# Kernel tuning notes

Measured on AMD Instinct MI355X. Metric: run time of the kernel, lower is better.

The kernel has to match this reference:

```python
import jax, jax.numpy as jnp
import numpy as np

VOCAB = 100000
EMB = 100
HID = 100
CTX_LEN = 60          # must equal MAX_DESC_LEN for linear_1 to fit
FACT_LEN = 20
DESC_LEN = 60


def setup_inputs() -> dict:
    key = jax.random.key(0)
    ks = jax.random.split(key, 12)
    s = 0.05
    context = jax.random.randint(ks[0], (CTX_LEN, FACT_LEN), 1, VOCAB)
    fact_lengths = jax.random.randint(ks[1], (CTX_LEN,), 1, FACT_LEN)
    description = jax.random.randint(ks[2], (DESC_LEN,), 1, VOCAB)
    emb_ctx = jax.random.normal(ks[3], (VOCAB, EMB), jnp.float32) * s
    emb_ctx = emb_ctx.at[0].set(0.0)  # padding_idx=0
    emb_dec = jax.random.normal(ks[4], (VOCAB, EMB), jnp.float32) * s
    emb_dec = emb_dec.at[0].set(0.0)
    w1 = jax.random.normal(ks[5], (HID, CTX_LEN * HID), jnp.float32) * s
    b1 = jax.random.normal(ks[6], (HID,), jnp.float32) * s
    w_ih = jax.random.normal(ks[7], (3 * HID, EMB), jnp.float32) * s
    w_hh = jax.random.normal(ks[8], (3 * HID, HID), jnp.float32) * s
    b_ih = jax.random.normal(ks[9], (3 * HID,), jnp.float32) * s
    b_hh = jax.random.normal(ks[10], (3 * HID,), jnp.float32) * s
    w_out = jax.random.normal(ks[11], (VOCAB, HID), jnp.float32) * s
    b_out = jnp.zeros((VOCAB,), jnp.float32)
    return {"context": context, "fact_lengths": fact_lengths, "description": description,
            "emb_ctx": emb_ctx, "emb_dec": emb_dec, "w1": w1, "b1": b1,
            "w_ih": w_ih, "w_hh": w_hh, "b_ih": b_ih, "b_hh": b_hh,
            "w_out": w_out, "b_out": b_out}


def _forward(context, description, emb_ctx, emb_dec, w1, b1,
             w_ih, w_hh, b_ih, b_hh, w_out, b_out):
    # ---- InputModule: embed + positional fact encoder ----
    emb = emb_ctx[context]                       # [CTX_LEN, FACT_LEN, EMB]
    slen, elen = FACT_LEN, EMB
    s = jnp.arange(slen, dtype=jnp.float32) / (slen - 1)   # [slen]
    e = jnp.arange(elen, dtype=jnp.float32) / (elen - 1)   # [elen]
    l = 1.0 - s[:, None] - e[None, :] * (1.0 - 2.0 * s[:, None])  # [slen, elen]
    facts = jnp.sum(emb * l[None], axis=1)       # [CTX_LEN, EMB]

    # ---- initial decoder hidden from flattened facts ----
    h0 = facts.reshape(1, -1) @ w1.T + b1        # [1, HID]

    x0 = emb_dec[1][None, :]                     # SOS token embedding [1, EMB]

    def step(carry, tok):
        h, x = carry
        gi = x @ w_ih.T + b_ih                   # [1, 3H]
        gh = h @ w_hh.T + b_hh
        i_r, i_z, i_n = jnp.split(gi, 3, axis=-1)
        h_r, h_z, h_n = jnp.split(gh, 3, axis=-1)
        r = jax.nn.sigmoid(i_r + h_r)
        z = jax.nn.sigmoid(i_z + h_z)
        n = jnp.tanh(i_n + r * h_n)
        h_new = (1.0 - z) * n + z * h            # [1, HID]
        logits = h_new @ w_out.T + b_out         # [1, VOCAB]
        logp = jax.nn.log_softmax(logits, axis=-1)
        loss_t = -logp[0, tok]                   # NLLLoss, batch 1
        x_next = emb_dec[tok][None, :]           # teacher forcing
        return (h_new, x_next), loss_t

    (_, _), losses = jax.lax.scan(step, (h0, x0), description)
    return jnp.sum(losses).reshape(1)            # matches torch FloatTensor([.])


def reference(context, fact_lengths, description, emb_ctx, emb_dec, w1, b1,
              w_ih, w_hh, b_ih, b_hh, w_out, b_out):
    # fact_lengths is unused by the original forward (PositionalFactEncoder ignores it)
    return _forward(context, description, emb_ctx, emb_dec, w1, b1,
                    w_ih, w_hh, b_ih, b_hh, w_out, b_out)
```

## Files before the change

### kernel.cpp

```cpp
#include <hip/hip_runtime.h>
#include <hip/hip_bf16.h>
#include <math.h>

#define VOCAB 100000
#define EMB 100
#define HID 100
#define CTX_LEN 60
#define FACT_LEN 20
#define DESC_LEN 60
#define NCHUNK (VOCAB / 16)
#define NWAVES 1024

#define WS_FACTS 0
#define WS_X     6000
#define WS_H0    12000
#define WS_GI    12160
#define WS_H     30160
#define WS_MS    36864

typedef __attribute__((ext_vector_type(8))) short short8;
typedef __attribute__((ext_vector_type(4))) float f32x4;

static __device__ __forceinline__ unsigned short f2bf(float f) {
    union { float f; unsigned u; } x; x.f = f;
    unsigned r = (x.u + 0x7FFFu + ((x.u >> 16) & 1u)) >> 16;
    return (unsigned short)r;
}

__global__ __launch_bounds__(128) void k1_prep(const int* __restrict__ context,
                                               const int* __restrict__ desc,
                                               const float* __restrict__ emb_ctx,
                                               const float* __restrict__ emb_dec,
                                               float* __restrict__ ws,
                                               float* __restrict__ out) {
    int b = blockIdx.x, tid = threadIdx.x;
    if (b < 60) {
        __shared__ int toks[20];
        if (tid < 20) toks[tid] = context[b * 20 + tid];
        __syncthreads();
        if (tid < 100) {
            float ef = tid * (1.f / 99.f);
            float acc = 0.f;
            #pragma unroll
            for (int s = 0; s < 20; s++) {
                float sf = s * (1.f / 19.f);
                float l = 1.f - sf - ef * (1.f - 2.f * sf);
                acc = fmaf(emb_ctx[toks[s] * 100 + tid], l, acc);
            }
            ws[WS_FACTS + b * 100 + tid] = acc;
        }
    } else {
        int t = b - 60;
        int tok = (t == 0) ? 1 : desc[t - 1];
        if (tid < 100) ws[WS_X + t * 100 + tid] = emb_dec[tok * 100 + tid];
        if (b == 60 && tid == 0) out[0] = 0.f;
    }
}

__global__ __launch_bounds__(320) void k2_h0_gi(const float* __restrict__ w1,
                                                const float* __restrict__ b1,
                                                const float* __restrict__ w_ih,
                                                const float* __restrict__ b_ih,
                                                float* __restrict__ ws) {
    int b = blockIdx.x, tid = threadIdx.x;
    if (b < 100) {
        __shared__ float red[320];
        const float* facts = ws + WS_FACTS;
        const float* wr = w1 + b * 6000;
        float p = 0.f;
        for (int k = tid; k < 6000; k += 320) p = fmaf(facts[k], wr[k], p);
        red[tid] = p; __syncthreads();
        if (tid < 64) red[tid] += red[256 + tid];
        __syncthreads();
        for (int st = 128; st > 0; st >>= 1) {
            if (tid < st) red[tid] += red[tid + st];
            __syncthreads();
        }
        if (tid == 0) ws[WS_H0 + b] = red[0] + b1[b];
    } else {
        int t = b - 100;
        __shared__ float xs[100];
        if (tid < 100) xs[tid] = ws[WS_X + t * 100 + tid];
        __syncthreads();
        if (tid < 300) {
            float p = b_ih[tid];
            const float* wr = w_ih + tid * 100;
            #pragma unroll 4
            for (int k = 0; k < 100; k++) p = fmaf(wr[k], xs[k], p);
            ws[WS_GI + t * 300 + tid] = p;
        }
    }
}

__global__ __launch_bounds__(320, 1) void k3_gru(const float* __restrict__ w_hh,
                                                 const float* __restrict__ b_hh,
                                                 float* __restrict__ ws) {
    __shared__ float gi_lds[18000];
    __shared__ float gh_lds[320];
    __shared__ __align__(16) unsigned short h_bf[128];

    const int tid = threadIdx.x;
    const int wave = tid >> 6, lane = tid & 63;
    const int q = lane >> 4, n = lane & 15;

    short8 bfr[16];
    #pragma unroll
    for (int i = 0; i < 4; i++) {
        int row = (wave * 4 + i) * 16 + n;
        const float* wr = w_hh + row * 100;
        #pragma unroll
        for (int kt = 0; kt < 4; kt++) {
            int k0 = kt * 32 + q * 8;
            float va[8];
            #pragma unroll
            for (int jj = 0; jj < 8; jj++) va[jj] = 0.f;
            if (row < 300) {
                if (k0 + 4 <= 100) {
                    float4 a = *(const float4*)(wr + k0);
                    va[0] = a.x; va[1] = a.y; va[2] = a.z; va[3] = a.w;
                }
                if (k0 + 8 <= 100) {
                    float4 b = *(const float4*)(wr + k0 + 4);
                    va[4] = b.x; va[5] = b.y; va[6] = b.z; va[7] = b.w;
                }
            }
            short8 f;
            #pragma unroll
            for (int jj = 0; jj < 8; jj++) f[jj] = (short)f2bf(va[jj]);
            bfr[i * 4 + kt] = f;
        }
    }

    for (int k = tid; k < 18000; k += 320) gi_lds[k] = ws[WS_GI + k];

    float hreg = 0.f, bh0 = 0.f, bh1 = 0.f, bh2 = 0.f;
    if (tid < 100) {
        hreg = ws[WS_H0 + tid];
        h_bf[tid] = f2bf(hreg);
        bh0 = b_hh[tid]; bh1 = b_hh[100 + tid]; bh2 = b_hh[200 + tid];
    } else if (tid < 128) {
        h_bf[tid] = 0;
    }
    __syncthreads();

    float* H = ws + WS_H;
    for (int t = 0; t < 60; t++) {
        short8 afr[4];
        #pragma unroll
        for (int kt = 0; kt < 4; kt++)
            afr[kt] = *(const short8*)&h_bf[kt * 32 + q * 8];
        #pragma unroll
        for (int i = 0; i < 4; i++) {
            f32x4 a = {0.f, 0.f, 0.f, 0.f};
            a = __builtin_amdgcn_mfma_f32_16x16x32_bf16(afr[0], bfr[i * 4 + 0], a, 0, 0, 0);
            a = __builtin_amdgcn_mfma_f32_16x16x32_bf16(afr[1], bfr[i * 4 + 1], a, 0, 0, 0);
            a = __builtin_amdgcn_mfma_f32_16x16x32_bf16(afr[2], bfr[i * 4 + 2], a, 0, 0, 0);
            a = __builtin_amdgcn_mfma_f32_16x16x32_bf16(afr[3], bfr[i * 4 + 3], a, 0, 0, 0);
            if (lane < 16) gh_lds[(wave * 4 + i) * 16 + lane] = a[0];
        }
        __syncthreads();
        if (tid < 100) {
            float gir = gi_lds[t * 300 + tid];
            float giz = gi_lds[t * 300 + 100 + tid];
            float gin = gi_lds[t * 300 + 200 + tid];
            float ghr = gh_lds[tid] + bh0;
            float ghz = gh_lds[100 + tid] + bh1;
            float ghn = gh_lds[200 + tid] + bh2;
            float r = 1.f / (1.f + __expf(-(gir + ghr)));
            float z = 1.f / (1.f + __expf(-(giz + ghz)));
            float a = fmaf(r, ghn, gin);
            float tt = __expf(-2.f * fabsf(a));
            float nn = copysignf((1.f - tt) / (1.f + tt), a);
            hreg = (1.f - z) * nn + z * hreg;
            h_bf[tid] = f2bf(hreg);
            H[t * 100 + tid] = hreg;
        }
        __syncthreads();
    }
}

__global__ __launch_bounds__(256, 1) void k4_logits(const float* __restrict__ w_out,
                                                    const float* __restrict__ b_out,
                                                    float* __restrict__ ws) {
    const float* H = ws + WS_H;
    float* ms = ws + WS_MS;
    const int lane = threadIdx.x & 63;
    const int gw = blockIdx.x * 4 + (threadIdx.x >> 6);
    const int q = lane >> 4, n = lane & 15;
    const int k_base = q * 8;

    short8 afr[4][4];
    #pragma unroll
    for (int mt = 0; mt < 4; mt++) {
        int m = mt * 16 + n;
        #pragma unroll
        for (int kt = 0; kt < 4; kt++) {
            int k0 = kt * 32 + k_base;
            float va[8];
            #pragma unroll
            for (int jj = 0; jj < 8; jj++) va[jj] = 0.f;
            if (m < 60) {
                if (k0 + 4 <= 100) {
                    float4 a = *(const float4*)(H + m * 100 + k0);
                    va[0] = a.x; va[1] = a.y; va[2] = a.z; va[3] = a.w;
                }
                if (k0 + 8 <= 100) {
                    float4 b = *(const float4*)(H + m * 100 + k0 + 4);
                    va[4] = b.x; va[5] = b.y; va[6] = b.z; va[7] = b.w;
                }
            }
            short8 f;
            #pragma unroll
            for (int jj = 0; jj < 8; jj++) f[jj] = (short)f2bf(va[jj]);
            afr[mt][kt] = f;
        }
    }

    float mS[16], sS[16];
    #pragma unroll
    for (int i = 0; i < 16; i++) { mS[i] = -3.0e38f; sS[i] = 0.f; }

    for (int c = gw; c < NCHUNK; c += NWAVES) {
        int row = c * 16 + n;
        short8 bfr[4];
        #pragma unroll
        for (int kt = 0; kt < 4; kt++) {
            int k0 = kt * 32 + k_base;
            float va[8];
            #pragma unroll
            for (int jj = 0; jj < 8; jj++) va[jj] = 0.f;
            if (k0 + 4 <= 100) {
                float4 a = *(const float4*)(w_out + row * 100 + k0);
                va[0] = a.x; va[1] = a.y; va[2] = a.z; va[3] = a.w;
            }
            if (k0 + 8 <= 100) {
                float4 b = *(const float4*)(w_out + row * 100 + k0 + 4);
                va[4] = b.x; va[5] = b.y; va[6] = b.z; va[7] = b.w;
            }
            short8 f;
            #pragma unroll
            for (int jj = 0; jj < 8; jj++) f[jj] = (short)f2bf(va[jj]);
            bfr[kt] = f;
        }
        float bo = b_out[row];
        #pragma unroll
        for (int mt = 0; mt < 4; mt++) {
            f32x4 acc = {0.f, 0.f, 0.f, 0.f};
            acc = __builtin_amdgcn_mfma_f32_16x16x32_bf16(afr[mt][0], bfr[0], acc, 0, 0, 0);
            acc = __builtin_amdgcn_mfma_f32_16x16x32_bf16(afr[mt][1], bfr[1], acc, 0, 0, 0);
            acc = __builtin_amdgcn_mfma_f32_16x16x32_bf16(afr[mt][2], bfr[2], acc, 0, 0, 0);
            acc = __builtin_amdgcn_mfma_f32_16x16x32_bf16(afr[mt][3], bfr[3], acc, 0, 0, 0);
            #pragma unroll
            for (int reg = 0; reg < 4; reg++) {
                float x = acc[reg] + bo;
                int i = mt * 4 + reg;
                float mo = mS[i];
                float mn = fmaxf(mo, x);
                sS[i] = sS[i] * __expf(mo - mn) + __expf(x - mn);
                mS[i] = mn;
            }
        }
    }

    #pragma unroll
    for (int i = 0; i < 16; i++) {
        float m = mS[i], s = sS[i];
        #pragma unroll
        for (int off = 1; off < 16; off <<= 1) {
            float m2 = __shfl_xor(m, off);
            float s2 = __shfl_xor(s, off);
            float mn = fmaxf(m, m2);
            s = s * __expf(m - mn) + s2 * __expf(m2 - mn);
            m = mn;
        }
        mS[i] = m; sS[i] = s;
    }
    if (n == 0) {
        #pragma unroll
        for (int mt = 0; mt < 4; mt++) {
            #pragma unroll
            for (int reg = 0; reg < 4; reg++) {
                int t = mt * 16 + q * 4 + reg;
                int i = mt * 4 + reg;
                if (t < 60) {
                    float2 val; val.x = mS[i]; val.y = sS[i];
                    ((float2*)ms)[t * NWAVES + gw] = val;
                }
            }
        }
    }
}

__global__ __launch_bounds__(256) void k5_final(const int* __restrict__ desc,
                                                const float* __restrict__ w_out,
                                                const float* __restrict__ b_out,
                                                const float* __restrict__ ws,
                                                float* __restrict__ out) {
    int t = blockIdx.x, tid = threadIdx.x;
    __shared__ float sm[256], ss[256], sd[256];
    const float2* ms = (const float2*)(ws + WS_MS);
    float m = -3.0e38f, s = 0.f;
    for (int i = tid; i < NWAVES; i += 256) {
        float2 p = ms[t * NWAVES + i];
        float mn = fmaxf(m, p.x);
        s = s * __expf(m - mn) + p.y * __expf(p.x - mn);
        m = mn;
    }
    sm[tid] = m; ss[tid] = s; __syncthreads();
    for (int st = 128; st > 0; st >>= 1) {
        if (tid < st) {
            float mo = sm[tid], so = ss[tid];
            float m2 = sm[tid + st], s2 = ss[tid + st];
            float mn = fmaxf(mo, m2);
            sm[tid] = mn;
            ss[tid] = so * __expf(mo - mn) + s2 * __expf(m2 - mn);
        }
        __syncthreads();
    }
    int tok = desc[t];
    float p = 0.f;
    if (tid < 100) p = ws[WS_H + t * 100 + tid] * w_out[tok * 100 + tid];
    sd[tid] = p; __syncthreads();
    for (int st = 128; st > 0; st >>= 1) {
        if (tid < st) sd[tid] += sd[tid + st];
        __syncthreads();
    }
    if (tid == 0) {
        float logit = sd[0] + b_out[tok];
        float loss = sm[0] + logf(ss[0]) - logit;
        atomicAdd(out, loss);
    }
}

extern "C" void kernel_launch(void* const* d_in, const int* in_sizes, int n_in,
                              void* d_out, int out_size, void* d_ws, size_t ws_size,
                              hipStream_t stream) {
    const int*   context = (const int*)d_in[0];
    const int*   desc    = (const int*)d_in[2];
    const float* emb_ctx = (const float*)d_in[3];
    const float* emb_dec = (const float*)d_in[4];
    const float* w1      = (const float*)d_in[5];
    const float* b1      = (const float*)d_in[6];
    const float* w_ih    = (const float*)d_in[7];
    const float* w_hh    = (const float*)d_in[8];
    const float* b_ih    = (const float*)d_in[9];
    const float* b_hh    = (const float*)d_in[10];
    const float* w_out   = (const float*)d_in[11];
    const float* b_out   = (const float*)d_in[12];
    float* out = (float*)d_out;
    float* ws  = (float*)d_ws;

    k1_prep  <<<120, 128, 0, stream>>>(context, desc, emb_ctx, emb_dec, ws, out);
    k2_h0_gi <<<160, 320, 0, stream>>>(w1, b1, w_ih, b_ih, ws);
    k3_gru   <<<1,   320, 0, stream>>>(w_hh, b_hh, ws);
    k4_logits<<<256, 256, 0, stream>>>(w_out, b_out, ws);
    k5_final <<<60,  256, 0, stream>>>(desc, w_out, b_out, ws, out);
}
```

Before: 204.9 us.

## Restructure GRU recurrence so each wave owns its gate rows, one barrier per step

The single-block GRU kernel now assigns each of 4 waves the r/z/n rows for the same 32 hidden units, so gate math reads MFMA accumulators directly from registers instead of going through a shared gh buffer. The hidden-state bf16 vector is double-buffered, which removes one of the two barriers per time step. Outputs H are staged in LDS and written out once at the end, and the gi preload uses float4 copies. This targets the serial latency of the 60-step recurrence, at the cost of more accumulator registers and some idle MFMA rows.

```diff
diff --git a/kernel.cpp b/kernel.cpp
--- a/kernel.cpp
+++ b/kernel.cpp
@@ -92,90 +92,115 @@
     }
 }
 
-__global__ __launch_bounds__(320, 1) void k3_gru(const float* __restrict__ w_hh,
+__global__ __launch_bounds__(256, 1) void k3_gru(const float* __restrict__ w_hh,
                                                  const float* __restrict__ b_hh,
                                                  float* __restrict__ ws) {
-    __shared__ float gi_lds[18000];
-    __shared__ float gh_lds[320];
-    __shared__ __align__(16) unsigned short h_bf[128];
+    __shared__ __align__(16) float gi_lds[18000];
+    __shared__ __align__(16) float H_lds[6000];
+    __shared__ __align__(16) unsigned short h_bf[2][128];
 
     const int tid = threadIdx.x;
     const int wave = tid >> 6, lane = tid & 63;
     const int q = lane >> 4, n = lane & 15;
-
-    short8 bfr[16];
+    const int L = lane & 31;
+    const int j = wave * 32 + L;
+    const bool gate_lane = (lane < 32) && (j < 100);
+
+    short8 bfr[3][2][4];
     #pragma unroll
-    for (int i = 0; i < 4; i++) {
-        int row = (wave * 4 + i) * 16 + n;
-        const float* wr = w_hh + row * 100;
-        #pragma unroll
-        for (int kt = 0; kt < 4; kt++) {
-            int k0 = kt * 32 + q * 8;
-            float va[8];
-            #pragma unroll
-            for (int jj = 0; jj < 8; jj++) va[jj] = 0.f;
-            if (row < 300) {
-                if (k0 + 4 <= 100) {
-                    float4 a = *(const float4*)(wr + k0);
-                    va[0] = a.x; va[1] = a.y; va[2] = a.z; va[3] = a.w;
+    for (int s = 0; s < 3; s++) {
+        #pragma unroll
+        for (int c = 0; c < 2; c++) {
+            const int jrow = wave * 32 + c * 16 + n;
+            const float* wr = w_hh + (s * 100 + jrow) * 100;
+            #pragma unroll
+            for (int kt = 0; kt < 4; kt++) {
+                int k0 = kt * 32 + q * 8;
+                float va[8];
+                #pragma unroll
+                for (int jj = 0; jj < 8; jj++) va[jj] = 0.f;
+                if (jrow < 100) {
+                    if (k0 + 4 <= 100) {
+                        float4 a = *(const float4*)(wr + k0);
+                        va[0] = a.x; va[1] = a.y; va[2] = a.z; va[3] = a.w;
+                    }
+                    if (k0 + 8 <= 100) {
+                        float4 b = *(const float4*)(wr + k0 + 4);
+                        va[4] = b.x; va[5] = b.y; va[6] = b.z; va[7] = b.w;
+                    }
                 }
-                if (k0 + 8 <= 100) {
-                    float4 b = *(const float4*)(wr + k0 + 4);
-                    va[4] = b.x; va[5] = b.y; va[6] = b.z; va[7] = b.w;
-                }
-            }
-            short8 f;
-            #pragma unroll
-            for (int jj = 0; jj < 8; jj++) f[jj] = (short)f2bf(va[jj]);
-            bfr[i * 4 + kt] = f;
-        }
-    }
-
-    for (int k = tid; k < 18000; k += 320) gi_lds[k] = ws[WS_GI + k];
+                short8 f;
+                #pragma unroll
+                for (int jj = 0; jj < 8; jj++) f[jj] = (short)f2bf(va[jj]);
+                bfr[s][c][kt] = f;
+            }
+        }
+    }
+
+    {
+        const float4* src = (const float4*)(ws + WS_GI);
+        float4* dst = (float4*)gi_lds;
+        for (int k = tid; k < 4500; k += 256) dst[k] = src[k];
+    }
 
     float hreg = 0.f, bh0 = 0.f, bh1 = 0.f, bh2 = 0.f;
-    if (tid < 100) {
-        hreg = ws[WS_H0 + tid];
-        h_bf[tid] = f2bf(hreg);
-        bh0 = b_hh[tid]; bh1 = b_hh[100 + tid]; bh2 = b_hh[200 + tid];
-    } else if (tid < 128) {
-        h_bf[tid] = 0;
+    if (gate_lane) {
+        hreg = ws[WS_H0 + j];
+        bh0 = b_hh[j]; bh1 = b_hh[100 + j]; bh2 = b_hh[200 + j];
+    }
+    if (tid < 128) {
+        h_bf[0][tid] = (tid < 100) ? f2bf(ws[WS_H0 + tid]) : (unsigned short)0;
+        h_bf[1][tid] = 0;
     }
     __syncthreads();
 
-    float* H = ws + WS_H;
+    const int js = (j < 100) ? j : 0;
     for (int t = 0; t < 60; t++) {
+        const int rb = t & 1;
+        float gir = gi_lds[t * 300 + js];
+        float giz = gi_lds[t * 300 + 100 + js];
+        float gin = gi_lds[t * 300 + 200 + js];
+
         short8 afr[4];
         #pragma unroll
         for (int kt = 0; kt < 4; kt++)
-            afr[kt] = *(const short8*)&h_bf[kt * 32 + q * 8];
-        #pragma unroll
-        for (int i = 0; i < 4; i++) {
-            f32x4 a = {0.f, 0.f, 0.f, 0.f};
-            a = __builtin_amdgcn_mfma_f32_16x16x32_bf16(afr[0], bfr[i * 4 + 0], a, 0, 0, 0);
-            a = __builtin_amdgcn_mfma_f32_16x16x32_bf16(afr[1], bfr[i * 4 + 1], a, 0, 0, 0);
-            a = __builtin_amdgcn_mfma_f32_16x16x32_bf16(afr[2], bfr[i * 4 + 2], a, 0, 0, 0);
-            a = __builtin_amdgcn_mfma_f32_16x16x32_bf16(afr[3], bfr[i * 4 + 3], a, 0, 0, 0);
-            if (lane < 16) gh_lds[(wave * 4 + i) * 16 + lane] = a[0];
-        }
-        __syncthreads();
-        if (tid < 100) {
-            float gir = gi_lds[t * 300 + tid];
-            float giz = gi_lds[t * 300 + 100 + tid];
-            float gin = gi_lds[t * 300 + 200 + tid];
-            float ghr = gh_lds[tid] + bh0;
-            float ghz = gh_lds[100 + tid] + bh1;
-            float ghn = gh_lds[200 + tid] + bh2;
+            afr[kt] = *(const short8*)&h_bf[rb][kt * 32 + q * 8];
+
+        f32x4 acc[3][2];
+        #pragma unroll
+        for (int s = 0; s < 3; s++) {
+            #pragma unroll
+            for (int c = 0; c < 2; c++) {
+                f32x4 a = {0.f, 0.f, 0.f, 0.f};
+                a = __builtin_amdgcn_mfma_f32_16x16x32_bf16(afr[0], bfr[s][c][0], a, 0, 0, 0);
+                a = __builtin_amdgcn_mfma_f32_16x16x32_bf16(afr[1], bfr[s][c][1], a, 0, 0, 0);
+                a = __builtin_amdgcn_mfma_f32_16x16x32_bf16(afr[2], bfr[s][c][2], a, 0, 0, 0);
+                a = __builtin_amdgcn_mfma_f32_16x16x32_bf16(afr[3], bfr[s][c][3], a, 0, 0, 0);
+                acc[s][c] = a;
+            }
+        }
+
+        if (gate_lane) {
+            const int cc = L >> 4;
+            float ghr = (cc ? acc[0][1][0] : acc[0][0][0]) + bh0;
+            float ghz = (cc ? acc[1][1][0] : acc[1][0][0]) + bh1;
+            float ghn = (cc ? acc[2][1][0] : acc[2][0][0]) + bh2;
             float r = 1.f / (1.f + __expf(-(gir + ghr)));
             float z = 1.f / (1.f + __expf(-(giz + ghz)));
-            float a = fmaf(r, ghn, gin);
-            float tt = __expf(-2.f * fabsf(a));
-            float nn = copysignf((1.f - tt) / (1.f + tt), a);
+            float a2 = fmaf(r, ghn, gin);
+            float tt = __expf(-2.f * fabsf(a2));
+            float nn = copysignf((1.f - tt) / (1.f + tt), a2);
             hreg = (1.f - z) * nn + z * hreg;
-            h_bf[tid] = f2bf(hreg);
-            H[t * 100 + tid] = hreg;
-        }
-        __syncthreads();
+            h_bf[rb ^ 1][j] = f2bf(hreg);
+            H_lds[t * 100 + j] = hreg;
+        }
+        __syncthreads();
+    }
+
+    {
+        const float4* src = (const float4*)H_lds;
+        float4* dst = (float4*)(ws + WS_H);
+        for (int k = tid; k < 1500; k += 256) dst[k] = src[k];
     }
 }
 
@@ -352,7 +377,7 @@
 
     k1_prep  <<<120, 128, 0, stream>>>(context, desc, emb_ctx, emb_dec, ws, out);
     k2_h0_gi <<<160, 320, 0, stream>>>(w1, b1, w_ih, b_ih, ws);
-    k3_gru   <<<1,   320, 0, stream>>>(w_hh, b_hh, ws);
+    k3_gru   <<<1,   256, 0, stream>>>(w_hh, b_hh, ws);
     k4_logits<<<256, 256, 0, stream>>>(w_out, b_out, ws);
     k5_final <<<60,  256, 0, stream>>>(desc, w_out, b_out, ws, out);
 }
```

New measurement: 200.3 us. 2.3% less time.
